# Kernel optimization log

Measured on AMD Instinct MI355X. Metric: run time of the kernel, lower is better.

Reference implementation:

```python
import jax, jax.numpy as jnp
import numpy as np

N_QUBITS = 10
N_LAYERS = 4
DIM = 2 ** N_QUBITS


def _apply_1q(state, gate, wire):
    """Apply a single-qubit gate on `wire` (wire 0 = most significant bit).

    state: (B, 2**n) complex64
    gate : (2, 2) shared across batch, or (B, 2, 2) per-sample.
    """
    B = state.shape[0]
    s = state.reshape(B, 2 ** wire, 2, -1)
    if gate.ndim == 2:
        s = jnp.einsum('ij,bxjy->bxiy', gate, s)
    else:
        s = jnp.einsum('bij,bxjy->bxiy', gate, s)
    return s.reshape(B, DIM)


def _apply_cnot(state, ctrl, tgt):
    """CNOT(ctrl, tgt): flip target amplitudes where control bit is 1."""
    B = state.shape[0]
    s = state.reshape((B,) + (2,) * N_QUBITS)
    s0 = jax.lax.index_in_dim(s, 0, 1 + ctrl, keepdims=True)
    s1 = jax.lax.index_in_dim(s, 1, 1 + ctrl, keepdims=True)
    s1 = jnp.flip(s1, axis=1 + tgt)
    s = jnp.concatenate([s0, s1], axis=1 + ctrl)
    return s.reshape(B, DIM)


def _rot_matrix(phi, theta, omega):
    """PennyLane Rot = RZ(omega) RY(theta) RZ(phi)."""
    c = jnp.cos(theta / 2).astype(jnp.complex64)
    s = jnp.sin(theta / 2).astype(jnp.complex64)
    ep = jnp.exp(-0.5j * (phi + omega).astype(jnp.complex64))   # e^{-i(phi+omega)/2}
    em = jnp.exp(-0.5j * (phi - omega).astype(jnp.complex64))   # e^{-i(phi-omega)/2}
    m00 = ep * c
    m01 = -jnp.conj(em) * s   # -e^{+i(phi-omega)/2} sin
    m10 = em * s
    m11 = jnp.conj(ep) * c    # e^{+i(phi+omega)/2} cos
    return jnp.array([[m00, m01], [m10, m11]], dtype=jnp.complex64)


def setup_inputs() -> dict:
    key = jax.random.key(0)
    k1, k2 = jax.random.split(key)
    inputs = jax.random.uniform(k1, (2048, N_QUBITS), dtype=jnp.float32)
    weights = 0.01 * jax.random.normal(k2, (N_LAYERS, N_QUBITS, 3), dtype=jnp.float32)
    return {"inputs": inputs, "weights": weights}


def reference(inputs, weights):
    B = inputs.shape[0]
    n = N_QUBITS
    # |0...0> batched state
    state = jnp.zeros((B, DIM), dtype=jnp.complex64).at[:, 0].set(1.0)

    # RX(pi * x_i) encoding (per-sample angles)
    for w in range(n):
        ang = jnp.pi * inputs[:, w]
        c = jnp.cos(ang / 2).astype(jnp.complex64)
        s = (-1j) * jnp.sin(ang / 2).astype(jnp.complex64)
        gate = jnp.stack([jnp.stack([c, s], -1),
                          jnp.stack([s, c], -1)], -2)  # (B, 2, 2)
        state = _apply_1q(state, gate, w)

    # StronglyEntanglingLayers: Rot on every wire, then CNOT ring with range r
    for l in range(N_LAYERS):
        for w in range(n):
            g = _rot_matrix(weights[l, w, 0], weights[l, w, 1], weights[l, w, 2])
            state = _apply_1q(state, g, w)
        r = (l % (n - 1)) + 1  # PennyLane default ranges
        for w in range(n):
            state = _apply_cnot(state, w, (w + r) % n)

    # <PauliZ> on last wire (least significant bit)
    probs = (state.real ** 2 + state.imag ** 2).reshape(B, -1, 2)
    z = jnp.sum(probs[:, :, 0] - probs[:, :, 1], axis=1)
    return z[:, None]
```

## Files before the change

kernel.cpp:

```cpp
#include <hip/hip_runtime.h>
#include <math.h>

#define NQ   10
#define NL   4
#define NREG 16
#define NPK  8

typedef float f32x2 __attribute__((ext_vector_type(2)));

struct MaskTab { int m[NL * NQ]; int d[NL * NQ]; bool keep[NL * NQ]; int sgn; bool ok; };

constexpr MaskTab make_masks() {
    MaskTab t{};
    int L[NQ] = {}, Li[NQ] = {};
    for (int p = 0; p < NQ; ++p) { L[p] = 1 << p; Li[p] = 1 << p; }
    for (int l = 0; l < NL; ++l) {
        for (int w = 0; w < NQ; ++w) {
            int p = NQ - 1 - w;
            int mm = 0;
            for (int tt = 0; tt < NQ; ++tt) mm |= ((Li[tt] >> p) & 1) << tt;
            t.m[l * NQ + w] = mm;
            t.d[l * NQ + w] = L[p];
        }
        int r = (l % (NQ - 1)) + 1;
        for (int w = 0; w < NQ; ++w) {
            int pc = NQ - 1 - w;
            int tq = w + r; if (tq >= NQ) tq -= NQ;
            int pt = NQ - 1 - tq;
            L[pt] ^= L[pc];
        }
        for (int w = 0; w < NQ; ++w) {
            int pc = NQ - 1 - w;
            int tq = w + r; if (tq >= NQ) tq -= NQ;
            int pt = NQ - 1 - tq;
            for (int p = 0; p < NQ; ++p)
                Li[p] ^= ((Li[p] >> pt) & 1) << pc;
        }
    }
    t.sgn = L[0];
    for (int gi = 0; gi < NL * NQ; ++gi) {
        if (gi < NQ) { t.keep[gi] = false; continue; }
        if (gi < (NL - 1) * NQ) { t.keep[gi] = true; continue; }
        t.keep[gi] = (__builtin_popcount((unsigned)(t.sgn & t.m[gi])) & 1) != 0;
    }
    bool ok = true;
    for (int p = 0; p < NQ; ++p) {
        int row = 0;
        for (int k = 0; k < NQ; ++k)
            if ((L[p] >> k) & 1) row ^= Li[k];
        if (row != (1 << p)) ok = false;
    }
    t.ok = ok;
    return t;
}

static constexpr MaskTab MK = make_masks();
static_assert(MK.ok, "GF(2) inverse check failed");

constexpr int dpp_direct(int m) {
    return m == 1 ? 0xB1 : m == 2 ? 0x4E : m == 3 ? 0x1B :
           m == 7 ? 0x141 : m == 8 ? 0x128 : m == 15 ? 0x140 : 0;
}
constexpr int dpp1(int m) {
    return dpp_direct(m)      ? dpp_direct(m) :
           dpp_direct(m ^ 8)  ? 0x128 :
           dpp_direct(m ^ 15) ? 0x140 : 0x141;
}
constexpr int dpp2(int m) {
    return dpp_direct(m)      ? 0 :
           dpp_direct(m ^ 8)  ? dpp_direct(m ^ 8) :
           dpp_direct(m ^ 15) ? dpp_direct(m ^ 15) : dpp_direct(m ^ 7);
}

template <int M>
__device__ __forceinline__ float xdpp(float v) {
    static_assert((M & ~15) == 0 && M != 0, "dpp mask must be 4-bit");
    int u = __builtin_amdgcn_mov_dpp(__float_as_int(v), dpp1(M), 0xF, 0xF, true);
    if constexpr (dpp2(M) != 0)
        u = __builtin_amdgcn_mov_dpp(u, dpp2(M), 0xF, 0xF, true);
    return __int_as_float(u);
}
template <int M>
__device__ __forceinline__ float xswz(float v) {
    static_assert((M & ~31) == 0 && M != 0, "swizzle mask must be 5-bit");
    return __int_as_float(__builtin_amdgcn_ds_swizzle(__float_as_int(v), (M << 10) | 0x1F));
}
__device__ __forceinline__ float xbp(int bpa, float v) {
    return __int_as_float(__builtin_amdgcn_ds_bpermute(bpa, __float_as_int(v)));
}

__device__ __forceinline__ float fxor(float a, unsigned s) {
    return __uint_as_float(__float_as_uint(a) ^ s);
}
__device__ __forceinline__ f32x2 bc2(float v) { f32x2 r; r.x = v; r.y = v; return r; }
__device__ __forceinline__ f32x2 swap2(f32x2 v) { f32x2 r; r.x = v.y; r.y = v.x; return r; }
__device__ __forceinline__ f32x2 cmul(f32x2 a, f32x2 b) {
    f32x2 r;
    r.x = a.x * b.x - a.y * b.y;
    r.y = a.x * b.y + a.y * b.x;
    return r;
}
__device__ __forceinline__ float rdl(float v, int l) {
    return __uint_as_float((unsigned)__builtin_amdgcn_readlane((int)__float_as_uint(v), l));
}

__device__ __forceinline__ void sincos_tiny(float a, float* s, float* c) {
    float t = a * a;
    *s = a * fmaf(t, fmaf(t, 8.3333333e-3f, -0.16666667f), 1.0f);
    *c = fmaf(t, fmaf(t, fmaf(t, -1.3888889e-3f, 4.1666668e-2f), -0.5f), 1.0f);
}
__device__ __forceinline__ void sincos_q(float a, float* s, float* c) {
    float h = 0.5f * a, u = h * h;
    float sh = h * fmaf(u, fmaf(u, fmaf(u, -1.9841270e-4f, 8.3333333e-3f), -0.16666667f), 1.0f);
    float ch = fmaf(u, fmaf(u, fmaf(u, fmaf(u, 2.4801587e-5f, -1.3888889e-3f),
                                    4.1666668e-2f), -0.5f), 1.0f);
    *s = 2.0f * sh * ch;
    *c = fmaf(-2.0f * sh, sh, 1.0f);
}

template <int GI>
__device__ __forceinline__ void apply_gate(f32x2 (&X)[NPK], f32x2 (&Y)[NPK],
                                           float g00x_r, float g00y_r,
                                           float g01x_r, float g01y_r, int lane) {
    if constexpr (MK.keep[GI]) {
        constexpr int m     = MK.m[GI];
        constexpr int d     = MK.d[GI];
        constexpr int mreg  = (m >> 6) & 15;
        constexpr int mlane = m & 63;
        constexpr int dreg  = (d >> 6) & 15;
        constexpr int dlane = d & 63;
        constexpr int  kreg  = mreg >> 1;
        constexpr bool kswap = (mreg & 1) != 0;
        constexpr bool useDPP = (mlane != 0) && ((mlane & 48) == 0);
        constexpr bool useSWZ = (mlane != 0) && !useDPP && ((mlane & 32) == 0);
        constexpr bool useBP  = (mlane != 0) && !useDPP && !useSWZ;

        const float g00x = rdl(g00x_r, GI);
        const float g00y = rdl(g00y_r, GI);
        const float g01x = rdl(g01x_r, GI);
        const float g01y = rdl(g01y_r, GI);

        const int bl = __popc(dlane & lane) & 1;
        const unsigned s0 = (unsigned)bl << 31;
        const float scy0 = fxor(g00y, s0), pcx0 = fxor(g01x, s0);
        const float scy1 = fxor(scy0, 0x80000000u), pcx1 = fxor(pcx0, 0x80000000u);

        f32x2 scyA, scyB, pcxA, pcxB;
        if constexpr (dreg & 1) {
            scyA.x = scy0; scyA.y = scy1;  scyB.x = scy1; scyB.y = scy0;
            pcxA.x = pcx0; pcxA.y = pcx1;  pcxB.x = pcx1; pcxB.y = pcx0;
        } else {
            scyA = bc2(scy0); scyB = bc2(scy1);
            pcxA = bc2(pcx0); pcxB = bc2(pcx1);
        }
        const f32x2 g00xv = bc2(g00x);
        const f32x2 g01yv = bc2(g01y);

        [[maybe_unused]] int bpa = 0;
        if constexpr (useBP) bpa = (lane ^ mlane) << 2;

        f32x2 pX[NPK], pY[NPK];
        #pragma unroll
        for (int k = 0; k < NPK; ++k) {
            f32x2 px = X[k ^ kreg], py = Y[k ^ kreg];
            if constexpr (kswap) { px = swap2(px); py = swap2(py); }
            if constexpr (useDPP) {
                px.x = xdpp<mlane & 15>(px.x); px.y = xdpp<mlane & 15>(px.y);
                py.x = xdpp<mlane & 15>(py.x); py.y = xdpp<mlane & 15>(py.y);
            } else if constexpr (useSWZ) {
                px.x = xswz<mlane & 31>(px.x); px.y = xswz<mlane & 31>(px.y);
                py.x = xswz<mlane & 31>(py.x); py.y = xswz<mlane & 31>(py.y);
            } else if constexpr (useBP) {
                px.x = xbp(bpa, px.x); px.y = xbp(bpa, px.y);
                py.x = xbp(bpa, py.x); py.y = xbp(bpa, py.y);
            }
            pX[k] = px; pY[k] = py;
        }
        #pragma unroll
        for (int k = 0; k < NPK; ++k) {
            const int vs = __popc(dreg & (2 * k)) & 1;
            const f32x2 scyv = vs ? scyB : scyA;
            const f32x2 pcxv = vs ? pcxB : pcxA;
            const f32x2 sX = X[k], sY = Y[k];
            f32x2 nX = sX * g00xv;
            nX -= scyv * sY;
            nX += pcxv * pX[k];
            nX -= g01yv * pY[k];
            f32x2 nY = sY * g00xv;
            nY += scyv * sX;
            nY += pcxv * pY[k];
            nY += g01yv * pX[k];
            X[k] = nX; Y[k] = nY;
        }
    }
}

template <int GI>
__device__ __forceinline__ void gates_from(f32x2 (&X)[NPK], f32x2 (&Y)[NPK],
                                           float g00x_r, float g00y_r,
                                           float g01x_r, float g01y_r, int lane) {
    if constexpr (GI < NL * NQ) {
        apply_gate<GI>(X, Y, g00x_r, g00y_r, g01x_r, g01y_r, lane);
        gates_from<GI + 1>(X, Y, g00x_r, g00y_r, g01x_r, g01y_r, lane);
    }
}

__global__ __launch_bounds__(64, 2) void qnn_kernel(const float* __restrict__ x,
                                                    const float* __restrict__ wts,
                                                    float* __restrict__ out) {
    const int b    = blockIdx.x;
    const int lane = threadIdx.x;

    const int gidx = (lane < NL * NQ) ? lane : 0;
    float g00x_r, g00y_r, g01x_r, g01y_r;
    {
        float phi = wts[gidx * 3 + 0];
        float th  = wts[gidx * 3 + 1];
        float om  = wts[gidx * 3 + 2];
        float st_, ct_; sincos_tiny(0.5f * th, &st_, &ct_);
        float sp,  cp;  sincos_tiny(0.5f * (phi + om), &sp, &cp);
        float sm,  cm;  sincos_tiny(0.5f * (phi - om), &sm, &cm);
        g00x_r =  cp * ct_;  g00y_r = -sp * ct_;
        g01x_r = -cm * st_;  g01y_r = -sm * st_;
    }

    float myc, mys;
    {
        const int w = (lane < NQ) ? lane : 0;
        sincos_q(1.57079632679f * x[b * NQ + w], &mys, &myc);
    }

    f32x2 u0[NQ], u1[NQ];
    #pragma unroll
    for (int w = 0; w < NQ; ++w) {
        const float a  = rdl(g00x_r, w), bb = rdl(g00y_r, w);
        const float c  = rdl(g01x_r, w), dd = rdl(g01y_r, w);
        const float cw = rdl(myc, w),    sw = rdl(mys, w);
        const int p = NQ - 1 - w;
        u0[p].x =  a * cw + dd * sw;
        u0[p].y = bb * cw -  c * sw;
        u1[p].x = -c * cw - bb * sw;
        u1[p].y = dd * cw -  a * sw;
    }

    f32x2 PL = (lane & 1) ? u1[0] : u0[0];
    #pragma unroll
    for (int p = 1; p < 6; ++p)
        PL = cmul(PL, ((lane >> p) & 1) ? u1[p] : u0[p]);

    f32x2 t67[4], r89[4];
    #pragma unroll
    for (int a = 0; a < 4; ++a) {
        f32x2 r = cmul((a & 1) ? u1[6] : u0[6], (a & 2) ? u1[7] : u0[7]);
        t67[a] = cmul(PL, r);
        r89[a] = cmul((a & 1) ? u1[8] : u0[8], (a & 2) ? u1[9] : u0[9]);
    }

    f32x2 X[NPK], Y[NPK];
    #pragma unroll
    for (int k = 0; k < NPK; ++k) {
        const int j0 = 2 * k, j1 = 2 * k + 1;
        f32x2 a0 = cmul(t67[j0 & 3], r89[j0 >> 2]);
        f32x2 a1 = cmul(t67[j1 & 3], r89[j1 >> 2]);
        X[k].x = a0.x; X[k].y = a1.x;
        Y[k].x = a0.y; Y[k].y = a1.y;
    }

    gates_from<NQ>(X, Y, g00x_r, g00y_r, g01x_r, g01y_r, lane);

    const int sl = __popc(MK.sgn & 63 & lane) & 1;
    const float bsign = sl ? -1.f : 1.f;
    const int sb = (MK.sgn >> 6) & 15;
    float acc = 0.f;
    #pragma unroll
    for (int k = 0; k < NPK; ++k) {
        const int c0 = __popc(sb & (2 * k)) & 1;
        const int c1 = c0 ^ (sb & 1);
        f32x2 mag = X[k] * X[k] + Y[k] * Y[k];
        acc = fmaf(mag.x, c0 ? -bsign : bsign, acc);
        acc = fmaf(mag.y, c1 ? -bsign : bsign, acc);
    }
    acc += xdpp<1>(acc);
    acc += xdpp<2>(acc);
    acc += xdpp<4>(acc);
    acc += xdpp<8>(acc);
    acc += xswz<16>(acc);
    acc += xbp((lane ^ 32) << 2, acc);
    if (lane == 0) out[b] = acc;
}

extern "C" void kernel_launch(void* const* d_in, const int* in_sizes, int n_in,
                              void* d_out, int out_size, void* d_ws, size_t ws_size,
                              hipStream_t stream) {
    (void)n_in; (void)d_ws; (void)ws_size; (void)out_size;
    const float* x   = (const float*)d_in[0];
    const float* wts = (const float*)d_in[1];
    float* out = (float*)d_out;
    int B = in_sizes[0] / NQ;
    qnn_kernel<<<B, 64, 0, stream>>>(x, wts, out);
}
```

Measured before the change: 18.06 us.

## Remap state amplitude layout via GF(2) basis change to cheapen cross-lane gate exchanges

Result: faster. 17.56 us (-2.8%).

```diff
diff --git a/kernel.cpp b/kernel.cpp
--- a/kernel.cpp
+++ b/kernel.cpp
@@ -3,7 +3,6 @@
 
 #define NQ   10
 #define NL   4
-#define NREG 16
 #define NPK  8
 
 typedef float f32x2 __attribute__((ext_vector_type(2)));
@@ -57,6 +56,129 @@
 static constexpr MaskTab MK = make_masks();
 static_assert(MK.ok, "GF(2) inverse check failed");
 
+struct Mat { unsigned c[10]; };
+
+constexpr unsigned mv(const Mat& M, unsigned v) {
+    unsigned r = 0;
+    for (int i = 0; i < 10; ++i) if ((v >> i) & 1u) r ^= M.c[i];
+    return r;
+}
+constexpr bool minvert(const Mat& A, Mat* out) {
+    unsigned rowA[10] = {}, rowI[10] = {};
+    for (int r = 0; r < 10; ++r) {
+        unsigned ra = 0;
+        for (int cc = 0; cc < 10; ++cc) ra |= ((A.c[cc] >> r) & 1u) << cc;
+        rowA[r] = ra; rowI[r] = 1u << r;
+    }
+    for (int col = 0; col < 10; ++col) {
+        int piv = -1;
+        for (int r = col; r < 10; ++r) if ((rowA[r] >> col) & 1u) { piv = r; break; }
+        if (piv < 0) return false;
+        unsigned ta = rowA[col]; rowA[col] = rowA[piv]; rowA[piv] = ta;
+        unsigned ti = rowI[col]; rowI[col] = rowI[piv]; rowI[piv] = ti;
+        for (int r = 0; r < 10; ++r)
+            if (r != col && ((rowA[r] >> col) & 1u)) { rowA[r] ^= rowA[col]; rowI[r] ^= rowI[col]; }
+    }
+    for (int cc = 0; cc < 10; ++cc) {
+        unsigned cv = 0;
+        for (int r = 0; r < 10; ++r) cv |= ((rowI[r] >> cc) & 1u) << r;
+        out->c[cc] = cv;
+    }
+    return true;
+}
+constexpr int xcost(unsigned m) {
+    unsigned ml = m & 63u;
+    if (ml == 0) return 0;
+    if ((ml & 48u) == 0) return 1;
+    if ((ml & 32u) == 0) return 3;
+    return 4;
+}
+
+struct Plan { Mat T, Ti; bool useT; int m[NL * NQ], d[NL * NQ], sgn; bool ok; };
+
+constexpr Plan make_plan() {
+    Plan P{};
+    P.ok = true;
+    unsigned dm[NL * NQ] = {}; int dmc[NL * NQ] = {}; int ndm = 0;
+    for (int gi = 0; gi < NL * NQ; ++gi) {
+        if (!MK.keep[gi]) continue;
+        unsigned m = (unsigned)MK.m[gi];
+        int f = -1;
+        for (int i = 0; i < ndm; ++i) if (dm[i] == m) { f = i; break; }
+        if (f < 0) { dm[ndm] = m; dmc[ndm] = xcost(m); ++ndm; }
+        else dmc[f] += xcost(m);
+    }
+    for (int i = 1; i < ndm; ++i) {
+        unsigned vm = dm[i]; int vc = dmc[i]; int j = i;
+        while (j > 0 && dmc[j - 1] < vc) { dm[j] = dm[j - 1]; dmc[j] = dmc[j - 1]; --j; }
+        dm[j] = vm; dmc[j] = vc;
+    }
+    unsigned sel[10] = {}; int nsel = 0;
+    unsigned gb[10] = {};
+    for (int i = 0; i < ndm && nsel < 9; ++i) {
+        unsigned r = dm[i];
+        for (int b = 9; b >= 0; --b) if (((r >> b) & 1u) && gb[b]) r ^= gb[b];
+        if (r == 0) continue;
+        int lb = 0;
+        for (int b = 9; b >= 0; --b) if ((r >> b) & 1u) { lb = b; break; }
+        gb[lb] = r;
+        sel[nsel++] = dm[i];
+    }
+    unsigned comp[10] = {}; int ncomp = 0;
+    for (int e = 0; e < 10 && nsel + ncomp < 10; ++e) {
+        unsigned r = 1u << e;
+        for (int b = 9; b >= 0; --b) if (((r >> b) & 1u) && gb[b]) r ^= gb[b];
+        if (r == 0) continue;
+        int lb = 0;
+        for (int b = 9; b >= 0; --b) if ((r >> b) & 1u) { lb = b; break; }
+        gb[lb] = r;
+        comp[ncomp++] = 1u << e;
+    }
+    if (nsel + ncomp != 10) { P.ok = false; return P; }
+    const unsigned tord[10] = {64, 128, 256, 512, 1, 2, 4, 8, 16, 32};
+    Mat S{}, Tt{};
+    for (int i = 0; i < 10; ++i) {
+        S.c[i]  = (i < nsel) ? sel[i] : comp[i - nsel];
+        Tt.c[i] = tord[i];
+    }
+    Mat Sinv{};
+    if (!minvert(S, &Sinv)) { P.ok = false; return P; }
+    for (int i = 0; i < 10; ++i) P.T.c[i] = mv(Tt, Sinv.c[i]);
+    if (!minvert(P.T, &P.Ti)) { P.ok = false; return P; }
+    for (int i = 0; i < 10; ++i) if (mv(P.T, P.Ti.c[i]) != (1u << i)) P.ok = false;
+    int cid = 0, cT = 0;
+    for (int gi = 0; gi < NL * NQ; ++gi) {
+        if (!MK.keep[gi]) continue;
+        cid += xcost((unsigned)MK.m[gi]);
+        cT  += xcost(mv(P.T, (unsigned)MK.m[gi]));
+    }
+    P.useT = (cT + 8 < cid);
+    for (int gi = 0; gi < NL * NQ; ++gi) {
+        if (P.useT) {
+            P.m[gi] = (int)mv(P.T, (unsigned)MK.m[gi]);
+            unsigned dd = 0;
+            for (int i = 0; i < 10; ++i)
+                dd |= (unsigned)(__builtin_popcount((unsigned)MK.d[gi] & P.Ti.c[i]) & 1) << i;
+            P.d[gi] = (int)dd;
+        } else { P.m[gi] = MK.m[gi]; P.d[gi] = MK.d[gi]; }
+    }
+    if (P.useT) {
+        unsigned ss = 0;
+        for (int i = 0; i < 10; ++i)
+            ss |= (unsigned)(__builtin_popcount((unsigned)MK.sgn & P.Ti.c[i]) & 1) << i;
+        P.sgn = (int)ss;
+    } else P.sgn = MK.sgn;
+    return P;
+}
+static constexpr Plan PLN = make_plan();
+static_assert(PLN.ok, "basis plan failed");
+
+constexpr unsigned kconstj(int j) {
+    unsigned r = 0;
+    for (int t = 0; t < 4; ++t) if ((j >> t) & 1) r ^= PLN.Ti.c[6 + t];
+    return r;
+}
+
 constexpr int dpp_direct(int m) {
     return m == 1 ? 0xB1 : m == 2 ? 0x4E : m == 3 ? 0x1B :
            m == 7 ? 0x141 : m == 8 ? 0x128 : m == 15 ? 0x140 : 0;
@@ -123,8 +245,8 @@
                                            float g00x_r, float g00y_r,
                                            float g01x_r, float g01y_r, int lane) {
     if constexpr (MK.keep[GI]) {
-        constexpr int m     = MK.m[GI];
-        constexpr int d     = MK.d[GI];
+        constexpr int m     = PLN.m[GI];
+        constexpr int d     = PLN.d[GI];
         constexpr int mreg  = (m >> 6) & 15;
         constexpr int mlane = m & 63;
         constexpr int dreg  = (d >> 6) & 15;
@@ -243,16 +365,16 @@
         u1[p].y = dd * cw -  a * sw;
     }
 
-    f32x2 PL = (lane & 1) ? u1[0] : u0[0];
+    f32x2 PLn = (lane & 1) ? u1[0] : u0[0];
     #pragma unroll
     for (int p = 1; p < 6; ++p)
-        PL = cmul(PL, ((lane >> p) & 1) ? u1[p] : u0[p]);
+        PLn = cmul(PLn, ((lane >> p) & 1) ? u1[p] : u0[p]);
 
     f32x2 t67[4], r89[4];
     #pragma unroll
     for (int a = 0; a < 4; ++a) {
         f32x2 r = cmul((a & 1) ? u1[6] : u0[6], (a & 2) ? u1[7] : u0[7]);
-        t67[a] = cmul(PL, r);
+        t67[a] = cmul(PLn, r);
         r89[a] = cmul((a & 1) ? u1[8] : u0[8], (a & 2) ? u1[9] : u0[9]);
     }
 
@@ -266,11 +388,39 @@
         Y[k].x = a0.y; Y[k].y = a1.y;
     }
 
+    if constexpr (PLN.useT) {
+        __shared__ float lb[2048];
+        #pragma unroll
+        for (int k = 0; k < NPK; ++k) {
+            #pragma unroll
+            for (int e = 0; e < 2; ++e) {
+                const int q = ((2 * k + e) << 6) | lane;
+                lb[2 * q]     = (e ? X[k].y : X[k].x);
+                lb[2 * q + 1] = (e ? Y[k].y : Y[k].x);
+            }
+        }
+        __syncthreads();
+        unsigned la = 0;
+        #pragma unroll
+        for (int i = 0; i < 6; ++i)
+            la ^= ((lane >> i) & 1) ? PLN.Ti.c[i] : 0u;
+        #pragma unroll
+        for (int k = 0; k < NPK; ++k) {
+            #pragma unroll
+            for (int e = 0; e < 2; ++e) {
+                const unsigned qs = la ^ kconstj(2 * k + e);
+                const float re = lb[2 * qs], im = lb[2 * qs + 1];
+                if (e) { X[k].y = re; Y[k].y = im; }
+                else   { X[k].x = re; Y[k].x = im; }
+            }
+        }
+    }
+
     gates_from<NQ>(X, Y, g00x_r, g00y_r, g01x_r, g01y_r, lane);
 
-    const int sl = __popc(MK.sgn & 63 & lane) & 1;
+    const int sl = __popc(PLN.sgn & 63 & lane) & 1;
     const float bsign = sl ? -1.f : 1.f;
-    const int sb = (MK.sgn >> 6) & 15;
+    const int sb = (PLN.sgn >> 6) & 15;
     float acc = 0.f;
     #pragma unroll
     for (int k = 0; k < NPK; ++k) {
```
